# Performance work log

Measured on AMD Instinct MI355X. Metric: run time of the kernel, lower is better.

Reference implementation:

```python
import jax, jax.numpy as jnp
import numpy as np

B = 8192; L = 50; D_EMB = 128
N_USER = 100000; N_MOVIE = 50000; N_DENSE = 8
D = 2 * D_EMB + D_EMB + N_DENSE  # 392 total_input_dim
E = 4; T = 2; H1 = 256; H2 = 128; ATT_H = 64; N_CROSS = 3


def setup_inputs() -> dict:
    key = jax.random.key(0)
    ks = jax.random.split(key, 28)
    rn = lambda k, shape, s=0.02: jax.random.normal(k, shape, jnp.float32) * s
    inp = {
        'userId': jax.random.randint(ks[0], (B,), 0, N_USER),
        'movieId': jax.random.randint(ks[1], (B,), 0, N_MOVIE),
        'seq_history': jax.random.randint(ks[2], (B, L), 0, N_MOVIE),
        'dense_feats': jax.random.normal(ks[3], (B, N_DENSE), jnp.float32),
        # embeddings (row 0 is padding_idx -> zeros)
        'emb_user': rn(ks[4], (N_USER + 1, D_EMB)).at[0].set(0.0),
        'emb_movie': rn(ks[5], (N_MOVIE + 1, D_EMB)).at[0].set(0.0),
        # DIN attention MLP: input [q,k,q-k,q*k] = 4*D_EMB
        'att_w1': rn(ks[6], (4 * D_EMB, ATT_H)), 'att_b1': jnp.zeros((ATT_H,), jnp.float32),
        'att_w2': rn(ks[7], (ATT_H, 1)), 'att_b2': jnp.zeros((1,), jnp.float32),
        # LayerNorms
        'in_gamma': jnp.ones((D,), jnp.float32), 'in_beta': jnp.zeros((D,), jnp.float32),
        'cr_gamma': jnp.ones((D,), jnp.float32), 'cr_beta': jnp.zeros((D,), jnp.float32),
        # CrossNetV2: x_{l+1} = x0 * (x_l W_l + b_l) + x_l
        'cross_W': rn(ks[8], (N_CROSS, D, D)), 'cross_b': jnp.zeros((N_CROSS, D), jnp.float32),
        # MMoE experts: Linear(D,H1)-ReLU-Linear(H1,H2), batched over E
        'exp_w1': rn(ks[9], (E, D, H1)), 'exp_b1': jnp.zeros((E, H1), jnp.float32),
        'exp_w2': rn(ks[10], (E, H1, H2)), 'exp_b2': jnp.zeros((E, H2), jnp.float32),
        # gates per task
        'gate_w': rn(ks[11], (T, D, E)), 'gate_b': jnp.zeros((T, E), jnp.float32),
        # task heads Linear(H2, 1)
        'head_w': rn(ks[12], (T, H2)), 'head_b': jnp.zeros((T,), jnp.float32),
    }
    return inp


def _layernorm(x, g, b, eps=1e-5):
    m = jnp.mean(x, axis=-1, keepdims=True)
    v = jnp.var(x, axis=-1, keepdims=True)
    return (x - m) * jax.lax.rsqrt(v + eps) * g + b


def _forward(userId, movieId, seq_history, dense_feats, emb_user, emb_movie,
             att_w1, att_b1, att_w2, att_b2, in_gamma, in_beta,
             cross_W, cross_b, cr_gamma, cr_beta,
             exp_w1, exp_b1, exp_w2, exp_b2, gate_w, gate_b, head_w, head_b):
    # sparse embedding gathers
    user_e = emb_user[userId]            # [B, D_EMB]
    movie_e = emb_movie[movieId]         # [B, D_EMB]  (target item)
    hist = emb_movie[seq_history]        # [B, L, D_EMB]
    mask = seq_history > 0               # [B, L]

    # DIN attention pooling
    q = jnp.broadcast_to(movie_e[:, None, :], hist.shape)            # [B, L, D_EMB]
    att_in = jnp.concatenate([q, hist, q - hist, q * hist], axis=-1)  # [B, L, 4*D_EMB]
    scores = (jax.nn.relu(att_in @ att_w1 + att_b1) @ att_w2 + att_b2)[..., 0]  # [B, L]
    scores = jnp.where(mask, scores, -1e9)
    probs = jax.nn.softmax(scores, axis=-1)                           # [B, L]
    interest = jnp.einsum('bl,bld->bd', probs, hist)                  # [B, D_EMB]

    x = jnp.concatenate([user_e, movie_e, interest, dense_feats], axis=-1)  # [B, D]
    x = _layernorm(x, in_gamma, in_beta)

    # CrossNetV2
    x0 = x
    for l in range(N_CROSS):
        x = x0 * (x @ cross_W[l] + cross_b[l]) + x
    x = _layernorm(x, cr_gamma, cr_beta)

    # MMoE: batched expert GEMMs + per-task soft gates
    h = jax.nn.relu(jnp.einsum('bd,edh->ebh', x, exp_w1) + exp_b1[:, None, :])  # [E,B,H1]
    eo = jnp.einsum('ebh,eho->ebo', h, exp_w2) + exp_b2[:, None, :]             # [E,B,H2]
    g = jax.nn.softmax(jnp.einsum('bd,tde->tbe', x, gate_w) + gate_b[:, None, :], axis=-1)  # [T,B,E]
    task_feat = jnp.einsum('tbe,ebo->tbo', g, eo)                                # [T,B,H2]

    logits = jnp.einsum('tbo,to->tb', task_feat, head_w) + head_b[:, None]       # [T,B]
    return logits


def reference(userId, movieId, seq_history, dense_feats, emb_user, emb_movie,
              att_w1, att_b1, att_w2, att_b2, in_gamma, in_beta,
              cross_W, cross_b, cr_gamma, cr_beta,
              exp_w1, exp_b1, exp_w2, exp_b2, gate_w, gate_b, head_w, head_b):
    return _forward(userId, movieId, seq_history, dense_feats, emb_user, emb_movie,
                    att_w1, att_b1, att_w2, att_b2, in_gamma, in_beta,
                    cross_W, cross_b, cr_gamma, cr_beta,
                    exp_w1, exp_b1, exp_w2, exp_b2, gate_w, gate_b, head_w, head_b)
```

## Files before the change

kernel.cpp:

```cpp
#include <hip/hip_runtime.h>
#include <hip/hip_bf16.h>

typedef short short8 __attribute__((ext_vector_type(8)));
typedef short short4v __attribute__((ext_vector_type(4)));
typedef float f32x4 __attribute__((ext_vector_type(4)));

constexpr int BB = 8192;
constexpr int LL = 50;
constexpr int DE = 128;
constexpr int DD = 392;
constexpr int HH1 = 256;
constexpr int HH2 = 128;

__device__ __forceinline__ short f2b(float x) {
    __hip_bfloat16 h = __float2bfloat16(x);
    return __builtin_bit_cast(short, h);
}
__device__ __forceinline__ float b2f(short v) {
    unsigned u = ((unsigned)(unsigned short)v) << 16;
    return __builtin_bit_cast(float, u);
}

__global__ __launch_bounds__(256) void prep_wqp(const float* __restrict__ w1,
                                                short* __restrict__ Wqpb) {
    int idx = blockIdx.x * 256 + threadIdx.x;
    Wqpb[idx] = f2b(w1[idx] + w1[idx + 16384]);
}

__global__ __launch_bounds__(256) void prep_wkwp(const float* __restrict__ w1,
                                                 short* __restrict__ WkFb,
                                                 short* __restrict__ WpFb) {
    int o = blockIdx.x * 256 + threadIdx.x;
    int e = o & 7, lane = (o >> 3) & 63, nt = (o >> 9) & 3, kt = o >> 11;
    int k = (kt << 5) + ((lane >> 4) << 3) + e;
    int h = (nt << 4) + (lane & 15);
    WkFb[o] = f2b(w1[(128 + k) * 64 + h] - w1[(256 + k) * 64 + h]);
    WpFb[o] = f2b(w1[(384 + k) * 64 + h]);
}

__global__ __launch_bounds__(256) void trans_kernel(const float* __restrict__ in,
                                                    short* __restrict__ out,
                                                    int R, int C) {
    long zo = (long)blockIdx.y * R * C;
    int idx = blockIdx.x * 256 + threadIdx.x;
    if (idx >= R * C) return;
    int c = idx / R, r = idx - c * R;
    out[zo + idx] = f2b(in[zo + (long)r * C + c]);
}

__global__ __launch_bounds__(256) void prep_hw2(const float* __restrict__ w2,
                                                const float* __restrict__ b2,
                                                const float* __restrict__ head_w,
                                                float* __restrict__ hw2,
                                                float* __restrict__ hc) {
    __shared__ float hw[256];
    const int e = blockIdx.x, t = threadIdx.x;
    hw[t] = head_w[t];
    __syncthreads();
    const float* row = &w2[((long)e * HH1 + t) * HH2];
    float s0 = 0.f, s1 = 0.f;
    #pragma unroll 8
    for (int o = 0; o < 128; o += 4) {
        float4 v = *reinterpret_cast<const float4*>(&row[o]);
        s0 += v.x * hw[o] + v.y * hw[o + 1] + v.z * hw[o + 2] + v.w * hw[o + 3];
        s1 += v.x * hw[128 + o] + v.y * hw[129 + o] + v.z * hw[130 + o] + v.w * hw[131 + o];
    }
    hw2[(((e << 8) + t) << 1) + 0] = s0;
    hw2[(((e << 8) + t) << 1) + 1] = s1;
    if (t < 2) {
        float s = 0.f;
        for (int o = 0; o < 128; ++o) s += b2[e * 128 + o] * hw[t * 128 + o];
        hc[e * 2 + t] = s;
    }
}

__global__ __launch_bounds__(256, 8) void attn_kernel(
    const int* __restrict__ userId, const int* __restrict__ movieId,
    const int* __restrict__ seq, const float* __restrict__ dense,
    const float* __restrict__ emb_user, const float* __restrict__ emb_movie,
    const short* __restrict__ Wqpb, const short* __restrict__ WkFb,
    const short* __restrict__ WpFb,
    const float* __restrict__ att_b1, const float* __restrict__ att_w2,
    const float* __restrict__ att_b2,
    const float* __restrict__ in_gamma, const float* __restrict__ in_beta,
    float* __restrict__ x0f, short* __restrict__ x0b)
{
    __shared__ short hist[64 * 128];
    __shared__ float qs[128];
    __shared__ int   seq_s[64];
    __shared__ float qconst[64];
    __shared__ float sp[4][64];
    __shared__ float probs[64];
    __shared__ float xrow[392];
    __shared__ float stats[2];

    const int b = blockIdx.x;
    const int t = threadIdx.x;
    const int lane = t & 63;
    const int w = t >> 6;

    if (t < 128) qs[t] = emb_movie[(long)movieId[b] * DE + t];
    if (t < 64)  seq_s[t] = (t < LL) ? seq[b * LL + t] : 0;
    __syncthreads();

    const int g  = t >> 5;
    const int d0 = (t & 31) << 2;
    #pragma unroll
    for (int i = 0; i < 8; ++i) {
        const int l = g + (i << 3);
        float4 v = make_float4(0.f, 0.f, 0.f, 0.f);
        if (l < LL)
            v = *reinterpret_cast<const float4*>(&emb_movie[(long)seq_s[l] * DE + d0]);
        short4v hv;
        hv[0] = f2b(v.x); hv[1] = f2b(v.y); hv[2] = f2b(v.z); hv[3] = f2b(v.w);
        const int byte = (l << 8) + ((d0 << 1) ^ ((l & 7) << 4));
        *reinterpret_cast<short4v*>(reinterpret_cast<char*>(hist) + byte) = hv;
    }

    float ue = (t < 128) ? emb_user[(long)userId[b] * DE + t] : 0.f;
    float dv = (t < 8) ? dense[b * 8 + t] : 0.f;

    short8 bfrag[4];
    #pragma unroll
    for (int kt = 0; kt < 4; ++kt) {
        const int fo = ((((kt << 2) + w) << 6) | lane) << 3;
        short8 wk = *reinterpret_cast<const short8*>(&WkFb[fo]);
        short8 wp = *reinterpret_cast<const short8*>(&WpFb[fo]);
        const int kq = (kt << 5) + ((lane >> 4) << 3);
        #pragma unroll
        for (int j = 0; j < 8; ++j)
            bfrag[kt][j] = f2b(fmaf(qs[kq + j], b2f(wp[j]), b2f(wk[j])));
    }

    {
        float s = 0.f;
        const int dq = w << 5;
        #pragma unroll
        for (int dd = 0; dd < 32; ++dd)
            s = fmaf(qs[dq + dd], b2f(Wqpb[(dq + dd) * 64 + lane]), s);
        sp[w][lane] = s;
    }
    __syncthreads();
    if (t < 64) qconst[t] = att_b1[t] + sp[0][t] + sp[1][t] + sp[2][t] + sp[3][t];
    __syncthreads();

    {
        const float qc  = qconst[(w << 4) + (lane & 15)];
        const float w2v = att_w2[(w << 4) + (lane & 15)];
        #pragma unroll
        for (int mt = 0; mt < 4; ++mt) {
            f32x4 acc;
            #pragma unroll
            for (int r = 0; r < 4; ++r) acc[r] = qc;
            const int row = (mt << 4) + (lane & 15);
            const int rbase = row << 8;
            const int swz = (row & 7) << 4;
            #pragma unroll
            for (int kt = 0; kt < 4; ++kt) {
                const int kbyte = (kt << 6) + ((lane >> 4) << 4);
                short8 a = *reinterpret_cast<const short8*>(
                    reinterpret_cast<char*>(hist) + rbase + (kbyte ^ swz));
                acc = __builtin_amdgcn_mfma_f32_16x16x32_bf16(a, bfrag[kt], acc, 0, 0, 0);
            }
            #pragma unroll
            for (int r = 0; r < 4; ++r) {
                float v = fmaxf(acc[r], 0.f) * w2v;
                v += __shfl_xor(v, 1); v += __shfl_xor(v, 2);
                v += __shfl_xor(v, 4); v += __shfl_xor(v, 8);
                if ((lane & 15) == 0)
                    sp[w][(mt << 4) + ((lane >> 4) << 2) + r] = v;
            }
        }
    }
    __syncthreads();

    if (t < 64) {
        float sc = sp[0][t] + sp[1][t] + sp[2][t] + sp[3][t] + att_b2[0];
        float s = (t < LL) ? ((seq_s[t] > 0) ? sc : -1e9f) : -INFINITY;
        float m = s;
        #pragma unroll
        for (int off = 32; off > 0; off >>= 1) m = fmaxf(m, __shfl_xor(m, off));
        float e = (t < LL) ? __expf(s - m) : 0.f;
        float sum = e;
        #pragma unroll
        for (int off = 32; off > 0; off >>= 1) sum += __shfl_xor(sum, off);
        probs[t] = (t < LL) ? (e / sum) : 0.f;
    }
    __syncthreads();

    float4 ps = make_float4(0.f, 0.f, 0.f, 0.f);
    #pragma unroll
    for (int i = 0; i < 8; ++i) {
        const int l = g + (i << 3);
        const int byte = (l << 8) + ((d0 << 1) ^ ((l & 7) << 4));
        short4v hv = *reinterpret_cast<const short4v*>(
            reinterpret_cast<const char*>(hist) + byte);
        const float p = probs[l];
        ps.x = fmaf(p, b2f(hv[0]), ps.x);
        ps.y = fmaf(p, b2f(hv[1]), ps.y);
        ps.z = fmaf(p, b2f(hv[2]), ps.z);
        ps.w = fmaf(p, b2f(hv[3]), ps.w);
    }
    ps.x += __shfl_xor(ps.x, 32); ps.y += __shfl_xor(ps.y, 32);
    ps.z += __shfl_xor(ps.z, 32); ps.w += __shfl_xor(ps.w, 32);
    __syncthreads();
    float* scr = reinterpret_cast<float*>(hist);
    if (lane < 32)
        *reinterpret_cast<float4*>(&scr[(w << 7) + ((lane & 31) << 2)]) = ps;
    __syncthreads();
    if (t < 128) {
        xrow[256 + t] = scr[t] + scr[128 + t] + scr[256 + t] + scr[384 + t];
        xrow[t] = ue;
        xrow[128 + t] = qs[t];
        if (t < 8) xrow[384 + t] = dv;
    }
    __syncthreads();

    float v0 = xrow[t];
    float v1 = (t < 136) ? xrow[256 + t] : 0.f;
    float s2 = v0 + v1, q2 = v0 * v0 + v1 * v1;
    #pragma unroll
    for (int off = 32; off > 0; off >>= 1) {
        s2 += __shfl_xor(s2, off);
        q2 += __shfl_xor(q2, off);
    }
    if (lane == 0) { sp[0][w] = s2; sp[1][w] = q2; }
    __syncthreads();
    if (t == 0) {
        float S = sp[0][0] + sp[0][1] + sp[0][2] + sp[0][3];
        float Q = sp[1][0] + sp[1][1] + sp[1][2] + sp[1][3];
        float mean = S / (float)DD;
        float var = Q / (float)DD - mean * mean;
        stats[0] = mean;
        stats[1] = rsqrtf(var + 1e-5f);
    }
    __syncthreads();
    const float mean = stats[0], inv = stats[1];
    const long base = (long)b * DD;
    float o0 = (v0 - mean) * inv * in_gamma[t] + in_beta[t];
    x0f[base + t] = o0; x0b[base + t] = f2b(o0);
    if (t < 136) {
        float o1 = (v1 - mean) * inv * in_gamma[256 + t] + in_beta[256 + t];
        x0f[base + 256 + t] = o1; x0b[base + 256 + t] = f2b(o1);
    }
}

template<int MODE, int WF32, int WB16, int NXB, int NZB>
__global__ __launch_bounds__(256) void bgemm(
    const short* __restrict__ A, const short* __restrict__ WT,
    const float* __restrict__ bias,
    float* __restrict__ outF, short* __restrict__ outB,
    const float* __restrict__ x0, const float* __restrict__ xin,
    int M, int N, int K, long aZ, long wZ, long bZ, long oZ)
{
    __shared__ short As[2][64 * 64];
    __shared__ short Bs[2][64 * 64];

    int id = blockIdx.x;
    const int qq = (int)gridDim.x >> 3;
    id = (id & 7) * qq + (id >> 3);
    const int mb  = id / (NXB * NZB);
    const int rem = id - mb * (NXB * NZB);
    const int z   = rem / NXB;
    const int xb  = rem - z * NXB;

    A += (long)z * aZ; WT += (long)z * wZ; bias += (long)z * bZ;
    const long oz = (long)z * oZ;

    const int t = threadIdx.x, w = t >> 6, lane = t & 63;
    const int m0 = mb * 64, n0 = xb * 64;
    const int sm = t >> 3, sk8 = (t & 7) << 3;

    f32x4 acc[4];
    #pragma unroll
    for (int i = 0; i < 4; ++i) {
        #pragma unroll
        for (int r = 0; r < 4; ++r) acc[i][r] = 0.f;
    }

    const int nsteps = (K + 63) >> 6;
    short8 avr[2], bvr[2];

    auto loadr = [&](int k0) {
        #pragma unroll
        for (int i = 0; i < 2; ++i) {
            const int r = sm + (i << 5);
            short8 zv = {0, 0, 0, 0, 0, 0, 0, 0};
            avr[i] = zv; bvr[i] = zv;
            if (k0 + sk8 < K) {
                avr[i] = *reinterpret_cast<const short8*>(&A[(long)(m0 + r) * K + k0 + sk8]);
                if (n0 + r < N)
                    bvr[i] = *reinterpret_cast<const short8*>(&WT[(long)(n0 + r) * K + k0 + sk8]);
            }
        }
    };
    auto writelds = [&](int buf) {
        #pragma unroll
        for (int i = 0; i < 2; ++i) {
            const int r = sm + (i << 5);
            const int byte = (r << 7) + ((sk8 << 1) ^ ((r & 7) << 4));
            *reinterpret_cast<short8*>(reinterpret_cast<char*>(&As[buf][0]) + byte) = avr[i];
            *reinterpret_cast<short8*>(reinterpret_cast<char*>(&Bs[buf][0]) + byte) = bvr[i];
        }
    };

    loadr(0);
    writelds(0);
    __syncthreads();

    int cur = 0;
    for (int s = 0; s < nsteps; ++s) {
        if (s + 1 < nsteps) loadr((s + 1) << 6);
        #pragma unroll
        for (int kt = 0; kt < 2; ++kt) {
            const int kbyte = (kt << 6) + ((lane >> 4) << 4);
            const int ar = (w << 4) + (lane & 15);
            short8 a = *reinterpret_cast<const short8*>(
                reinterpret_cast<char*>(&As[cur][0]) + (ar << 7) + (kbyte ^ ((ar & 7) << 4)));
            #pragma unroll
            for (int nt = 0; nt < 4; ++nt) {
                const int br = (nt << 4) + (lane & 15);
                short8 bb = *reinterpret_cast<const short8*>(
                    reinterpret_cast<char*>(&Bs[cur][0]) + (br << 7) + (kbyte ^ ((br & 7) << 4)));
                acc[nt] = __builtin_amdgcn_mfma_f32_16x16x32_bf16(a, bb, acc[nt], 0, 0, 0);
            }
        }
        if (s + 1 < nsteps) writelds(cur ^ 1);
        __syncthreads();
        cur ^= 1;
    }

    #pragma unroll
    for (int nt = 0; nt < 4; ++nt) {
        const int col = n0 + (nt << 4) + (lane & 15);
        if (col < N) {
            const float bv = bias[col];
            #pragma unroll
            for (int r = 0; r < 4; ++r) {
                const int row = m0 + (w << 4) + ((lane >> 4) << 2) + r;
                float v = acc[nt][r] + bv;
                if (MODE == 1) v = fmaxf(v, 0.f);
                const long o = (long)row * N + col;
                if (MODE == 2) v = x0[o] * v + xin[o];
                if (WF32) outF[oz + o] = v;
                if (WB16) outB[oz + o] = f2b(v);
            }
        }
    }
}

__global__ __launch_bounds__(256) void ln_kernel(
    const float* __restrict__ in,
    const float* __restrict__ gamma, const float* __restrict__ beta,
    float* __restrict__ outF, short* __restrict__ outB)
{
    __shared__ float red[2][4];
    __shared__ float stats[2];
    const int b = blockIdx.x, t = threadIdx.x, lane = t & 63, w = t >> 6;
    const long base = (long)b * DD;
    float v0 = in[base + t];
    float v1 = (t < 136) ? in[base + 256 + t] : 0.f;
    float s = v0 + v1, q2 = v0 * v0 + v1 * v1;
    #pragma unroll
    for (int off = 32; off > 0; off >>= 1) {
        s += __shfl_xor(s, off);
        q2 += __shfl_xor(q2, off);
    }
    if (lane == 0) { red[0][w] = s; red[1][w] = q2; }
    __syncthreads();
    if (t == 0) {
        float S = red[0][0] + red[0][1] + red[0][2] + red[0][3];
        float Q = red[1][0] + red[1][1] + red[1][2] + red[1][3];
        float mean = S / (float)DD;
        float var = Q / (float)DD - mean * mean;
        stats[0] = mean;
        stats[1] = rsqrtf(var + 1e-5f);
    }
    __syncthreads();
    const float mean = stats[0], inv = stats[1];
    float o0 = (v0 - mean) * inv * gamma[t] + beta[t];
    outF[base + t] = o0; outB[base + t] = f2b(o0);
    if (t < 136) {
        float o1 = (v1 - mean) * inv * gamma[256 + t] + beta[256 + t];
        outF[base + 256 + t] = o1; outB[base + 256 + t] = f2b(o1);
    }
}

__global__ __launch_bounds__(256) void final_kernel(
    const float* __restrict__ x, const short* __restrict__ h1,
    const float* __restrict__ hw2, const float* __restrict__ hc,
    const float* __restrict__ gate_w, const float* __restrict__ gate_b,
    const float* __restrict__ head_b, float* __restrict__ out)
{
    const int t = threadIdx.x, lane = t & 63, w = t >> 6;
    const int b = blockIdx.x * 4 + w;
    const float* xr = x + (long)b * DD;

    float xv[7];
    #pragma unroll
    for (int i = 0; i < 7; ++i) {
        int d = lane + (i << 6);
        xv[i] = (d < DD) ? xr[d] : 0.f;
    }

    float gl[8] = {0.f, 0.f, 0.f, 0.f, 0.f, 0.f, 0.f, 0.f};
    #pragma unroll
    for (int i = 0; i < 7; ++i) {
        int d = lane + (i << 6);
        if (d < DD) {
            float4 g0 = *reinterpret_cast<const float4*>(&gate_w[d << 2]);
            float4 g1 = *reinterpret_cast<const float4*>(&gate_w[1568 + (d << 2)]);
            gl[0] = fmaf(xv[i], g0.x, gl[0]); gl[1] = fmaf(xv[i], g0.y, gl[1]);
            gl[2] = fmaf(xv[i], g0.z, gl[2]); gl[3] = fmaf(xv[i], g0.w, gl[3]);
            gl[4] = fmaf(xv[i], g1.x, gl[4]); gl[5] = fmaf(xv[i], g1.y, gl[5]);
            gl[6] = fmaf(xv[i], g1.z, gl[6]); gl[7] = fmaf(xv[i], g1.w, gl[7]);
        }
    }

    float ed[8];
    #pragma unroll
    for (int e = 0; e < 4; ++e) {
        short4v hv = *reinterpret_cast<const short4v*>(
            &h1[((long)e * BB + b) * HH1 + (lane << 2)]);
        const float* hwp = &hw2[(((e << 8) + (lane << 2))) << 1];
        float4 w01 = *reinterpret_cast<const float4*>(hwp);
        float4 w23 = *reinterpret_cast<const float4*>(hwp + 4);
        float h0 = b2f(hv[0]), h1f = b2f(hv[1]), h2 = b2f(hv[2]), h3 = b2f(hv[3]);
        ed[e]     = fmaf(h0, w01.x, fmaf(h1f, w01.z, fmaf(h2, w23.x, h3 * w23.z)));
        ed[4 + e] = fmaf(h0, w01.y, fmaf(h1f, w01.w, fmaf(h2, w23.y, h3 * w23.w)));
    }

    #pragma unroll
    for (int v = 0; v < 8; ++v) {
        #pragma unroll
        for (int off = 32; off > 0; off >>= 1) {
            gl[v] += __shfl_xor(gl[v], off);
            ed[v] += __shfl_xor(ed[v], off);
        }
    }

    if (lane == 0) {
        float res[2];
        #pragma unroll
        for (int tt = 0; tt < 2; ++tt) {
            float lv[4], m = -1e30f;
            #pragma unroll
            for (int e = 0; e < 4; ++e) {
                lv[e] = gl[tt * 4 + e] + gate_b[tt * 4 + e];
                m = fmaxf(m, lv[e]);
            }
            float sum = 0.f, acc = 0.f;
            #pragma unroll
            for (int e = 0; e < 4; ++e) { lv[e] = __expf(lv[e] - m); sum += lv[e]; }
            #pragma unroll
            for (int e = 0; e < 4; ++e)
                acc = fmaf(lv[e], ed[tt * 4 + e] + hc[e * 2 + tt], acc);
            res[tt] = head_b[tt] + acc / sum;
        }
        out[b] = res[0];
        out[BB + b] = res[1];
    }
}

extern "C" void kernel_launch(void* const* d_in, const int* in_sizes, int n_in,
                              void* d_out, int out_size, void* d_ws, size_t ws_size,
                              hipStream_t stream) {
    const int*   userId    = (const int*)d_in[0];
    const int*   movieId   = (const int*)d_in[1];
    const int*   seq       = (const int*)d_in[2];
    const float* dense     = (const float*)d_in[3];
    const float* emb_user  = (const float*)d_in[4];
    const float* emb_movie = (const float*)d_in[5];
    const float* att_w1    = (const float*)d_in[6];
    const float* att_b1    = (const float*)d_in[7];
    const float* att_w2    = (const float*)d_in[8];
    const float* att_b2    = (const float*)d_in[9];
    const float* in_gamma  = (const float*)d_in[10];
    const float* in_beta   = (const float*)d_in[11];
    const float* cr_gamma  = (const float*)d_in[12];
    const float* cr_beta   = (const float*)d_in[13];
    const float* cross_W   = (const float*)d_in[14];
    const float* cross_b   = (const float*)d_in[15];
    const float* exp_w1    = (const float*)d_in[16];
    const float* exp_b1    = (const float*)d_in[17];
    const float* exp_w2    = (const float*)d_in[18];
    const float* exp_b2    = (const float*)d_in[19];
    const float* gate_w    = (const float*)d_in[20];
    const float* gate_b    = (const float*)d_in[21];
    const float* head_w    = (const float*)d_in[22];
    const float* head_b    = (const float*)d_in[23];
    float* outp = (float*)d_out;

    char* p = (char*)d_ws;
    auto alloc = [&](size_t bytes) -> char* {
        char* r = p; p += (bytes + 255) & ~(size_t)255; return r;
    };
    short* Wqpb = (short*)alloc(8192 * 2);
    short* WkFb = (short*)alloc(8192 * 2);
    short* WpFb = (short*)alloc(8192 * 2);
    float* hw2 = (float*)alloc(2048 * 4);
    float* hc  = (float*)alloc(8 * 4);
    short* WTc = (short*)alloc((size_t)3 * 392 * 392 * 2);
    short* WT1 = (short*)alloc((size_t)4 * 256 * 392 * 2);
    float* x0f = (float*)alloc((size_t)BB * DD * 4);
    short* x0b = (short*)alloc((size_t)BB * DD * 2);
    float* xAf = (float*)alloc((size_t)BB * DD * 4);
    short* xAb = (short*)alloc((size_t)BB * DD * 2);
    float* xBf = (float*)alloc((size_t)BB * DD * 4);
    short* xBb = (short*)alloc((size_t)BB * DD * 2);
    short* h1b = (short*)alloc((size_t)4 * BB * HH1 * 2);

    prep_wqp<<<32, 256, 0, stream>>>(att_w1, Wqpb);
    prep_wkwp<<<32, 256, 0, stream>>>(att_w1, WkFb, WpFb);
    trans_kernel<<<dim3(601, 3), 256, 0, stream>>>(cross_W, WTc, 392, 392);
    trans_kernel<<<dim3(392, 4), 256, 0, stream>>>(exp_w1, WT1, 392, 256);
    prep_hw2<<<4, 256, 0, stream>>>(exp_w2, exp_b2, head_w, hw2, hc);

    attn_kernel<<<BB, 256, 0, stream>>>(userId, movieId, seq, dense,
                                        emb_user, emb_movie, Wqpb, WkFb, WpFb,
                                        att_b1, att_w2, att_b2,
                                        in_gamma, in_beta, x0f, x0b);

    bgemm<2, 1, 1, 7, 1><<<896, 256, 0, stream>>>(x0b, WTc, cross_b, xAf, xAb,
                                                  x0f, x0f, BB, DD, DD, 0, 0, 0, 0);
    bgemm<2, 1, 1, 7, 1><<<896, 256, 0, stream>>>(xAb, WTc + 392 * 392, cross_b + 392,
                                                  xBf, xBb, x0f, xAf, BB, DD, DD, 0, 0, 0, 0);
    bgemm<2, 1, 0, 7, 1><<<896, 256, 0, stream>>>(xBb, WTc + 2 * 392 * 392, cross_b + 784,
                                                  xAf, nullptr, x0f, xBf, BB, DD, DD, 0, 0, 0, 0);

    ln_kernel<<<BB, 256, 0, stream>>>(xAf, cr_gamma, cr_beta, xBf, xBb);

    bgemm<1, 0, 1, 4, 4><<<2048, 256, 0, stream>>>(
        xBb, WT1, exp_b1, nullptr, h1b, nullptr, nullptr,
        BB, HH1, DD, 0, (long)HH1 * DD, HH1, (long)BB * HH1);

    final_kernel<<<BB / 4, 256, 0, stream>>>(xBf, h1b, hw2, hc,
                                             gate_w, gate_b, head_b, outp);

    (void)in_sizes; (void)n_in; (void)out_size; (void)ws_size;
}
```

Measured before the change: 189.8 us.

## Pre-convert movie embedding table to bf16 and merge prep kernels

Result: faster. 175.1 us (-7.8%).

```diff
diff --git a/kernel.cpp b/kernel.cpp
--- a/kernel.cpp
+++ b/kernel.cpp
@@ -21,56 +21,72 @@
     return __builtin_bit_cast(float, u);
 }
 
-__global__ __launch_bounds__(256) void prep_wqp(const float* __restrict__ w1,
-                                                short* __restrict__ Wqpb) {
+__global__ __launch_bounds__(256) void prep_small(
+    const float* __restrict__ w1,
+    const float* __restrict__ w2, const float* __restrict__ b2,
+    const float* __restrict__ head_w,
+    short* __restrict__ Wqpb, short* __restrict__ WkFb, short* __restrict__ WpFb,
+    float* __restrict__ hw2, float* __restrict__ hc)
+{
+    __shared__ float hw[256];
+    const int b = blockIdx.x, t = threadIdx.x;
+    if (b < 32) {
+        int idx = b * 256 + t;
+        Wqpb[idx] = f2b(w1[idx] + w1[idx + 16384]);
+    } else if (b < 64) {
+        int o = (b - 32) * 256 + t;
+        int e = o & 7, lane = (o >> 3) & 63, nt = (o >> 9) & 3, kt = o >> 11;
+        int k = (kt << 5) + ((lane >> 4) << 3) + e;
+        int h = (nt << 4) + (lane & 15);
+        WkFb[o] = f2b(w1[(128 + k) * 64 + h] - w1[(256 + k) * 64 + h]);
+        WpFb[o] = f2b(w1[(384 + k) * 64 + h]);
+    } else {
+        const int e = b - 64;
+        hw[t] = head_w[t];
+        __syncthreads();
+        const float* row = &w2[((long)e * HH1 + t) * HH2];
+        float s0 = 0.f, s1 = 0.f;
+        #pragma unroll 8
+        for (int o = 0; o < 128; o += 4) {
+            float4 v = *reinterpret_cast<const float4*>(&row[o]);
+            s0 += v.x * hw[o] + v.y * hw[o + 1] + v.z * hw[o + 2] + v.w * hw[o + 3];
+            s1 += v.x * hw[128 + o] + v.y * hw[129 + o] + v.z * hw[130 + o] + v.w * hw[131 + o];
+        }
+        hw2[(((e << 8) + t) << 1) + 0] = s0;
+        hw2[(((e << 8) + t) << 1) + 1] = s1;
+        if (t < 2) {
+            float s = 0.f;
+            for (int o = 0; o < 128; ++o) s += b2[e * 128 + o] * hw[t * 128 + o];
+            hc[e * 2 + t] = s;
+        }
+    }
+}
+
+constexpr int S0 = 3 * 392 * 392;
+constexpr int S1 = 4 * 392 * 256;
+constexpr int S2 = (50001 * 128) / 4;
+
+__global__ __launch_bounds__(256) void prep_trans(
+    const float* __restrict__ cross_W, const float* __restrict__ exp_w1,
+    const float* __restrict__ emb_movie,
+    short* __restrict__ WTc, short* __restrict__ WT1, short* __restrict__ embB)
+{
     int idx = blockIdx.x * 256 + threadIdx.x;
-    Wqpb[idx] = f2b(w1[idx] + w1[idx + 16384]);
-}
-
-__global__ __launch_bounds__(256) void prep_wkwp(const float* __restrict__ w1,
-                                                 short* __restrict__ WkFb,
-                                                 short* __restrict__ WpFb) {
-    int o = blockIdx.x * 256 + threadIdx.x;
-    int e = o & 7, lane = (o >> 3) & 63, nt = (o >> 9) & 3, kt = o >> 11;
-    int k = (kt << 5) + ((lane >> 4) << 3) + e;
-    int h = (nt << 4) + (lane & 15);
-    WkFb[o] = f2b(w1[(128 + k) * 64 + h] - w1[(256 + k) * 64 + h]);
-    WpFb[o] = f2b(w1[(384 + k) * 64 + h]);
-}
-
-__global__ __launch_bounds__(256) void trans_kernel(const float* __restrict__ in,
-                                                    short* __restrict__ out,
-                                                    int R, int C) {
-    long zo = (long)blockIdx.y * R * C;
-    int idx = blockIdx.x * 256 + threadIdx.x;
-    if (idx >= R * C) return;
-    int c = idx / R, r = idx - c * R;
-    out[zo + idx] = f2b(in[zo + (long)r * C + c]);
-}
-
-__global__ __launch_bounds__(256) void prep_hw2(const float* __restrict__ w2,
-                                                const float* __restrict__ b2,
-                                                const float* __restrict__ head_w,
-                                                float* __restrict__ hw2,
-                                                float* __restrict__ hc) {
-    __shared__ float hw[256];
-    const int e = blockIdx.x, t = threadIdx.x;
-    hw[t] = head_w[t];
-    __syncthreads();
-    const float* row = &w2[((long)e * HH1 + t) * HH2];
-    float s0 = 0.f, s1 = 0.f;
-    #pragma unroll 8
-    for (int o = 0; o < 128; o += 4) {
-        float4 v = *reinterpret_cast<const float4*>(&row[o]);
-        s0 += v.x * hw[o] + v.y * hw[o + 1] + v.z * hw[o + 2] + v.w * hw[o + 3];
-        s1 += v.x * hw[128 + o] + v.y * hw[129 + o] + v.z * hw[130 + o] + v.w * hw[131 + o];
-    }
-    hw2[(((e << 8) + t) << 1) + 0] = s0;
-    hw2[(((e << 8) + t) << 1) + 1] = s1;
-    if (t < 2) {
-        float s = 0.f;
-        for (int o = 0; o < 128; ++o) s += b2[e * 128 + o] * hw[t * 128 + o];
-        hc[e * 2 + t] = s;
+    if (idx < S0) {
+        int z = idx / (392 * 392), rr = idx - z * 392 * 392;
+        int c = rr / 392, r = rr - c * 392;
+        WTc[idx] = f2b(cross_W[(long)z * 153664 + r * 392 + c]);
+    } else if (idx < S0 + S1) {
+        int j = idx - S0;
+        int z = j / 100352, rr = j - z * 100352;
+        int c = rr / 392, r = rr - c * 392;
+        WT1[j] = f2b(exp_w1[(long)z * 100352 + r * 256 + c]);
+    } else if (idx < S0 + S1 + S2) {
+        long j = (long)(idx - S0 - S1) << 2;
+        float4 v = *reinterpret_cast<const float4*>(&emb_movie[j]);
+        short4v o;
+        o[0] = f2b(v.x); o[1] = f2b(v.y); o[2] = f2b(v.z); o[3] = f2b(v.w);
+        *reinterpret_cast<short4v*>(&embB[j]) = o;
     }
 }
 
@@ -78,6 +94,7 @@
     const int* __restrict__ userId, const int* __restrict__ movieId,
     const int* __restrict__ seq, const float* __restrict__ dense,
     const float* __restrict__ emb_user, const float* __restrict__ emb_movie,
+    const short* __restrict__ embB,
     const short* __restrict__ Wqpb, const short* __restrict__ WkFb,
     const short* __restrict__ WpFb,
     const float* __restrict__ att_b1, const float* __restrict__ att_w2,
@@ -103,18 +120,13 @@
     if (t < 64)  seq_s[t] = (t < LL) ? seq[b * LL + t] : 0;
     __syncthreads();
 
-    const int g  = t >> 5;
-    const int d0 = (t & 31) << 2;
-    #pragma unroll
-    for (int i = 0; i < 8; ++i) {
-        const int l = g + (i << 3);
-        float4 v = make_float4(0.f, 0.f, 0.f, 0.f);
-        if (l < LL)
-            v = *reinterpret_cast<const float4*>(&emb_movie[(long)seq_s[l] * DE + d0]);
-        short4v hv;
-        hv[0] = f2b(v.x); hv[1] = f2b(v.y); hv[2] = f2b(v.z); hv[3] = f2b(v.w);
-        const int byte = (l << 8) + ((d0 << 1) ^ ((l & 7) << 4));
-        *reinterpret_cast<short4v*>(reinterpret_cast<char*>(hist) + byte) = hv;
+    #pragma unroll
+    for (int i = 0; i < 4; ++i) {
+        const int idx = t + (i << 8);
+        const int l = idx >> 4, c = idx & 15;
+        short8 hv = *reinterpret_cast<const short8*>(&embB[(long)seq_s[l] * DE + (c << 3)]);
+        const int byte = (l << 8) + ((c << 4) ^ ((l & 7) << 4));
+        *reinterpret_cast<short8*>(reinterpret_cast<char*>(hist) + byte) = hv;
     }
 
     float ue = (t < 128) ? emb_user[(long)userId[b] * DE + t] : 0.f;
@@ -188,6 +200,8 @@
     }
     __syncthreads();
 
+    const int g  = t >> 5;
+    const int d0 = (t & 31) << 2;
     float4 ps = make_float4(0.f, 0.f, 0.f, 0.f);
     #pragma unroll
     for (int i = 0; i < 8; ++i) {
@@ -502,6 +516,7 @@
     float* hc  = (float*)alloc(8 * 4);
     short* WTc = (short*)alloc((size_t)3 * 392 * 392 * 2);
     short* WT1 = (short*)alloc((size_t)4 * 256 * 392 * 2);
+    short* embB = (short*)alloc((size_t)50001 * 128 * 2);
     float* x0f = (float*)alloc((size_t)BB * DD * 4);
     short* x0b = (short*)alloc((size_t)BB * DD * 2);
     float* xAf = (float*)alloc((size_t)BB * DD * 4);
@@ -510,14 +525,14 @@
     short* xBb = (short*)alloc((size_t)BB * DD * 2);
     short* h1b = (short*)alloc((size_t)4 * BB * HH1 * 2);
 
-    prep_wqp<<<32, 256, 0, stream>>>(att_w1, Wqpb);
-    prep_wkwp<<<32, 256, 0, stream>>>(att_w1, WkFb, WpFb);
-    trans_kernel<<<dim3(601, 3), 256, 0, stream>>>(cross_W, WTc, 392, 392);
-    trans_kernel<<<dim3(392, 4), 256, 0, stream>>>(exp_w1, WT1, 392, 256);
-    prep_hw2<<<4, 256, 0, stream>>>(exp_w2, exp_b2, head_w, hw2, hc);
+    prep_small<<<68, 256, 0, stream>>>(att_w1, exp_w2, exp_b2, head_w,
+                                       Wqpb, WkFb, WpFb, hw2, hc);
+    prep_trans<<<(S0 + S1 + S2 + 255) / 256, 256, 0, stream>>>(
+        cross_W, exp_w1, emb_movie, WTc, WT1, embB);
 
     attn_kernel<<<BB, 256, 0, stream>>>(userId, movieId, seq, dense,
-                                        emb_user, emb_movie, Wqpb, WkFb, WpFb,
+                                        emb_user, emb_movie, embB,
+                                        Wqpb, WkFb, WpFb,
                                         att_b1, att_w2, att_b2,
                                         in_gamma, in_beta, x0f, x0b);
 
```
